# Optimization experiments

Measured on AMD Instinct MI355X. Metric: run time of the kernel, lower is better.

## Reference

```python
import jax, jax.numpy as jnp
import numpy as np

IN_FEATURES = 512
OUT_FEATURES = 512
GRID_SIZE = 8
SPLINE_ORDER = 3


def make_grid():
    # grid has grid_size + 2*spline_order + 1 knots in [-1, 1]
    return jnp.linspace(-1.0, 1.0, GRID_SIZE + 2 * SPLINE_ORDER + 1, dtype=jnp.float32)


def b_splines(x, grid):
    # x: (N, in)  ->  bases: (N, in, grid_size + spline_order)
    x = jnp.clip(x, -2.0, 2.0)[..., None]  # (N, in, 1)
    bases = ((x >= grid[:-1]) & (x < grid[1:])).astype(x.dtype)
    for k in range(1, SPLINE_ORDER + 1):
        denom1 = grid[k:-1] - grid[:-(k + 1)]
        denom1 = jnp.where(jnp.abs(denom1) < 1e-8, jnp.ones_like(denom1), denom1)
        denom2 = grid[k + 1:] - grid[1:-k]
        denom2 = jnp.where(jnp.abs(denom2) < 1e-8, jnp.ones_like(denom2), denom2)
        bases = ((x - grid[:-(k + 1)]) / denom1 * bases[..., :-1]
                 + (grid[k + 1:] - x) / denom2 * bases[..., 1:])
    return bases


def setup_inputs() -> dict:
    key = jax.random.key(0)
    kx, kb, ks = jax.random.split(key, 3)
    x = jax.random.normal(kx, (8192, IN_FEATURES), dtype=jnp.float32)
    # xavier_uniform with gain=0.5 for base_weight
    limit = 0.5 * np.sqrt(6.0 / (IN_FEATURES + OUT_FEATURES))
    base_weight = jax.random.uniform(kb, (OUT_FEATURES, IN_FEATURES), dtype=jnp.float32,
                                     minval=-limit, maxval=limit)
    spline_weight = 0.01 * jax.random.normal(
        ks, (OUT_FEATURES, IN_FEATURES, GRID_SIZE + SPLINE_ORDER), dtype=jnp.float32)
    return {"x": x, "base_weight": base_weight, "spline_weight": spline_weight}


def reference(x, base_weight, spline_weight):
    grid = make_grid()
    base_out = x @ base_weight.T                      # (N, out)
    basis = b_splines(x, grid)                        # (N, in, G+K)
    spline_out = jnp.einsum('bij,oij->bo', basis, spline_weight)
    return base_out + spline_out
```

## Files before the change

kernel.cpp:

```cpp
#include <hip/hip_runtime.h>
#include <stdint.h>

#define IN_F 512
#define OUT_F 512
#define NROWS 8192
#define NSLOT 12
#define KTOT (IN_F * NSLOT)
#define K16S (KTOT / 16)
#define SW_ROW (IN_F * 11)
#define KC_PAD 776
#define AROW 120
#define NGRP 32

typedef __bf16 bf16x8 __attribute__((ext_vector_type(8)));
typedef __bf16 bf16x2 __attribute__((ext_vector_type(2)));
typedef float f32x16 __attribute__((ext_vector_type(16)));

__device__ ushort g_Wb[(K16S * 16 + 1) * 512];

__device__ __forceinline__ ushort f2bf(float f) {
    uint32_t u = __builtin_bit_cast(uint32_t, f);
    u += 0x7FFFu + ((u >> 16) & 1u);
    return (ushort)(u >> 16);
}

__global__ __launch_bounds__(256) void prep_weights(const float* __restrict__ bw,
                                                    const float* __restrict__ sw) {
    __shared__ __align__(16) ushort kcol[16 * KC_PAD];
    const int t  = threadIdx.x;
    const int nt = blockIdx.x & 15;
    const int kg = (blockIdx.x >> 4) & 7;
    const int hv = blockIdx.x >> 7;
    const int o0 = nt * 32 + hv * 16;
    const int f0 = kg * 64;

    {
        const int o_l = t >> 4;
        const int tr  = t & 15;
        const float* swr = sw + (size_t)(o0 + o_l) * SW_ROW + (size_t)f0 * 11;
        #pragma unroll
        for (int i = 0; i < 11; ++i) {
            int p4 = tr + i * 16;
            float4 v = ((const float4*)swr)[p4];
            uint pos = (uint)p4 * 4;
            #pragma unroll
            for (int c = 0; c < 4; ++c) {
                uint pc = pos + c;
                uint fl = pc / 11u;
                uint j  = pc - fl * 11u;
                float val = (c == 0) ? v.x : (c == 1) ? v.y : (c == 2) ? v.z : v.w;
                kcol[o_l * KC_PAD + fl * NSLOT + j] = f2bf(val);
            }
        }
        #pragma unroll
        for (int i = 0; i < 4; ++i) {
            int fl = tr * 4 + i;
            kcol[o_l * KC_PAD + fl * NSLOT + 11] =
                f2bf(bw[(size_t)(o0 + o_l) * IN_F + f0 + fl]);
        }
    }
    __syncthreads();

    {
        const int ol16 = t & 15;
        const int ch   = t >> 4;
        #pragma unroll
        for (int i = 0; i < 6; ++i) {
            int idx  = ch + i * 16;
            int k16l = idx >> 1;
            int hf   = idx & 1;
            uint4 val = *(const uint4*)&kcol[ol16 * KC_PAD + k16l * 16 + hf * 8];
            ((uint4*)g_Wb)[((size_t)nt * K16S + kg * 48 + k16l) * 64 + hf * 32 + hv * 16 + ol16] = val;
        }
    }
}

__device__ __forceinline__ void eval12(float xx, uint p[6]) {
    float wpos = (xx + 1.0f) * 7.0f;
    float fi = floorf(wpos);
    int   i  = (int)fi;
    float u  = wpos - fi;
    bool inr = (xx >= -1.0f) && (xx < 1.0f);
    int   q  = i - 3;
    float um = 1.0f - u;
    float uu = u * u, u3 = uu * u;
    const float C6 = 1.0f / 6.0f;
    float s0 = (inr && q >= 0) ? C6 : 0.0f;
    float s1 = (inr && q >= -1 && q <= 9) ? C6 : 0.0f;
    float s2 = (inr && q >= -2 && q <= 8) ? C6 : 0.0f;
    float s3 = (inr && q <= 7) ? C6 : 0.0f;
    float b0 = um * um * um * s0;
    float b1 = fmaf(3.0f, u3, fmaf(-6.0f, uu, 4.0f)) * s1;
    float b2 = fmaf(-3.0f, u3, fmaf(3.0f, uu, fmaf(3.0f, u, 1.0f))) * s2;
    float b3 = u3 * s3;
    bf16x2 k01; k01[0] = (__bf16)b0; k01[1] = (__bf16)b1;
    bf16x2 k23; k23[0] = (__bf16)b2; k23[1] = (__bf16)b3;
    uint K01 = __builtin_bit_cast(uint, k01);
    uint K23 = __builtin_bit_cast(uint, k23);
    int r  = q & 1;
    int e0 = q & ~1;
    uint P0 = r ? (K01 << 16) : K01;
    uint P1 = r ? ((K01 >> 16) | (K23 << 16)) : K23;
    uint P2 = r ? (K23 >> 16) : 0u;
    #pragma unroll
    for (int pi = 0; pi < 6; ++pi) {
        int d = 2 * pi - e0;
        p[pi] = (d == 0) ? P0 : (d == 2) ? P1 : (d == 4) ? P2 : 0u;
    }
    p[5] = (p[5] & 0xFFFFu) | ((uint)f2bf(xx) << 16);
}

__device__ __forceinline__ void stage4(float4 xv, ushort* dst) {
    uint p[4][6];
    eval12(xv.x, p[0]);
    eval12(xv.y, p[1]);
    eval12(xv.z, p[2]);
    eval12(xv.w, p[3]);
    uint4* d4 = (uint4*)dst;
    d4[0] = make_uint4(p[0][0], p[0][1], p[0][2], p[0][3]);
    d4[1] = make_uint4(p[0][4], p[0][5], p[1][0], p[1][1]);
    d4[2] = make_uint4(p[1][2], p[1][3], p[1][4], p[1][5]);
    d4[3] = make_uint4(p[2][0], p[2][1], p[2][2], p[2][3]);
    d4[4] = make_uint4(p[2][4], p[2][5], p[3][0], p[3][1]);
    d4[5] = make_uint4(p[3][2], p[3][3], p[3][4], p[3][5]);
}

__global__ __launch_bounds__(256, 2) void kan_gemm(const float* __restrict__ x,
                                                   float* __restrict__ out) {
    __shared__ __align__(16) ushort As[2][128 * AROW];

    const int t    = threadIdx.x;
    const int lane = t & 63;
    const int wv   = t >> 6;
    const int wr   = wv >> 1;
    const int wc   = wv & 1;
    const int ln31 = lane & 31;
    const int half = lane >> 5;

    const int bx = blockIdx.x;
    const int mb = bx >> 3;
    const int cg = (bx >> 1) & 3;
    const int kp = bx & 1;
    const int row_base = mb * 128;

    const int srow = t >> 1;
    const int fq   = t & 1;
    const float* xp = x + (size_t)(row_base + srow) * IN_F + kp * 256 + fq * 4;
    ushort* const sb0 = &As[0][srow * AROW + fq * 48];
    ushort* const sb1 = &As[1][srow * AROW + fq * 48];

    const int ntg0 = cg * 4 + wc * 2;
    const uint4* Bp0 = (const uint4*)g_Wb + ((size_t)ntg0 * K16S + kp * 192) * 64 + lane;
    const uint4* Bp1 = Bp0 + (size_t)K16S * 64;

    f32x16 acc[2][2] = {};

    float4 xv = *(const float4*)xp;
    stage4(xv, sb0);
    float4 xn = *(const float4*)(xp + 8);
    __syncthreads();

    #pragma unroll 1
    for (int g = 0; g < NGRP; ++g) {
        const int cur = g & 1;
        uint4 breg[6][2];
        #pragma unroll
        for (int ks = 0; ks < 6; ++ks) {
            breg[ks][0] = Bp0[(size_t)(g * 6 + ks) * 64];
            breg[ks][1] = Bp1[(size_t)(g * 6 + ks) * 64];
        }
        const int gf = (g + 2 < NGRP) ? g + 2 : (NGRP - 1);
        float4 xf = *(const float4*)(xp + gf * 8);

        if (g + 1 < NGRP) stage4(xn, cur ? sb0 : sb1);

        const ushort* Ac = As[cur];
        #pragma unroll
        for (int ks = 0; ks < 6; ++ks) {
            uint4 a0 = *(const uint4*)&Ac[(wr * 64 + ln31) * AROW + ks * 16 + half * 8];
            uint4 a1 = *(const uint4*)&Ac[(wr * 64 + 32 + ln31) * AROW + ks * 16 + half * 8];
            bf16x8 af0 = __builtin_bit_cast(bf16x8, a0);
            bf16x8 af1 = __builtin_bit_cast(bf16x8, a1);
            bf16x8 bf0 = __builtin_bit_cast(bf16x8, breg[ks][0]);
            bf16x8 bf1 = __builtin_bit_cast(bf16x8, breg[ks][1]);
            acc[0][0] = __builtin_amdgcn_mfma_f32_32x32x16_bf16(af0, bf0, acc[0][0], 0, 0, 0);
            acc[0][1] = __builtin_amdgcn_mfma_f32_32x32x16_bf16(af0, bf1, acc[0][1], 0, 0, 0);
            acc[1][0] = __builtin_amdgcn_mfma_f32_32x32x16_bf16(af1, bf0, acc[1][0], 0, 0, 0);
            acc[1][1] = __builtin_amdgcn_mfma_f32_32x32x16_bf16(af1, bf1, acc[1][1], 0, 0, 0);
        }

        xn = xf;
        __syncthreads();
    }

    #pragma unroll
    for (int mt = 0; mt < 2; ++mt) {
        #pragma unroll
        for (int nt = 0; nt < 2; ++nt) {
            int rb = row_base + wr * 64 + mt * 32 + 4 * half;
            int cc = cg * 128 + wc * 64 + nt * 32 + ln31;
            #pragma unroll
            for (int reg = 0; reg < 16; ++reg) {
                int rr = rb + (reg & 3) + 8 * (reg >> 2);
                unsafeAtomicAdd(&out[(size_t)rr * OUT_F + cc], acc[mt][nt][reg]);
            }
        }
    }
}

extern "C" void kernel_launch(void* const* d_in, const int* in_sizes, int n_in,
                              void* d_out, int out_size, void* d_ws, size_t ws_size,
                              hipStream_t stream) {
    const float* x  = (const float*)d_in[0];
    const float* bw = (const float*)d_in[1];
    const float* sw = (const float*)d_in[2];
    float* out = (float*)d_out;
    hipMemsetAsync(out, 0, (size_t)out_size * sizeof(float), stream);
    hipLaunchKernelGGL(prep_weights, dim3(256), dim3(256), 0, stream, bw, sw);
    hipLaunchKernelGGL(kan_gemm, dim3(512), dim3(256), 0, stream, x, out);
}
```

Baseline: 170.8 us.

## Split K four ways, single-buffer A tile, fold output zeroing into prep

Raises the split-K factor from 2 to 4, so the GEMM grid doubles to 1024 blocks, each covering 16 K-groups. The A tile drops from double to single buffering, which halves LDS use and lets the launch bound ask for 3 blocks per CU. The cost is two barriers per iteration with no overlap between staging and MFMA. The output memset moves into the prep kernel to save a separate launch, but doubling split-K also doubles the atomic adds to the output.

Result: faster. 165.9 us (-2.8%).

```diff
diff --git a/kernel.cpp b/kernel.cpp
--- a/kernel.cpp
+++ b/kernel.cpp
@@ -10,7 +10,6 @@
 #define SW_ROW (IN_F * 11)
 #define KC_PAD 776
 #define AROW 120
-#define NGRP 32
 
 typedef __bf16 bf16x8 __attribute__((ext_vector_type(8)));
 typedef __bf16 bf16x2 __attribute__((ext_vector_type(2)));
@@ -25,14 +24,23 @@
 }
 
 __global__ __launch_bounds__(256) void prep_weights(const float* __restrict__ bw,
-                                                    const float* __restrict__ sw) {
+                                                    const float* __restrict__ sw,
+                                                    float* __restrict__ out) {
     __shared__ __align__(16) ushort kcol[16 * KC_PAD];
     const int t  = threadIdx.x;
-    const int nt = blockIdx.x & 15;
-    const int kg = (blockIdx.x >> 4) & 7;
-    const int hv = blockIdx.x >> 7;
+    const int b  = blockIdx.x;
+    const int nt = b & 15;
+    const int kg = (b >> 4) & 7;
+    const int hv = b >> 7;
     const int o0 = nt * 32 + hv * 16;
     const int f0 = kg * 64;
+
+    {
+        float4* o4 = (float4*)out;
+        const float4 z = make_float4(0.f, 0.f, 0.f, 0.f);
+        #pragma unroll
+        for (int i = 0; i < 16; ++i) o4[(size_t)b * 4096 + i * 256 + t] = z;
+    }
 
     {
         const int o_l = t >> 4;
@@ -116,18 +124,20 @@
     eval12(xv.y, p[1]);
     eval12(xv.z, p[2]);
     eval12(xv.w, p[3]);
-    uint4* d4 = (uint4*)dst;
-    d4[0] = make_uint4(p[0][0], p[0][1], p[0][2], p[0][3]);
-    d4[1] = make_uint4(p[0][4], p[0][5], p[1][0], p[1][1]);
-    d4[2] = make_uint4(p[1][2], p[1][3], p[1][4], p[1][5]);
-    d4[3] = make_uint4(p[2][0], p[2][1], p[2][2], p[2][3]);
-    d4[4] = make_uint4(p[2][4], p[2][5], p[3][0], p[3][1]);
-    d4[5] = make_uint4(p[3][2], p[3][3], p[3][4], p[3][5]);
-}
-
-__global__ __launch_bounds__(256, 2) void kan_gemm(const float* __restrict__ x,
+    #pragma unroll
+    for (int c = 0; c < 4; ++c) {
+        uint2 w0; w0.x = p[c][0]; w0.y = p[c][1];
+        uint2 w1; w1.x = p[c][2]; w1.y = p[c][3];
+        uint2 w2; w2.x = p[c][4]; w2.y = p[c][5];
+        *(uint2*)&dst[c * 12 + 0] = w0;
+        *(uint2*)&dst[c * 12 + 4] = w1;
+        *(uint2*)&dst[c * 12 + 8] = w2;
+    }
+}
+
+__global__ __launch_bounds__(256, 3) void kan_gemm(const float* __restrict__ x,
                                                    float* __restrict__ out) {
-    __shared__ __align__(16) ushort As[2][128 * AROW];
+    __shared__ __align__(16) ushort As[128 * AROW];
 
     const int t    = threadIdx.x;
     const int lane = t & 63;
@@ -138,47 +148,44 @@
     const int half = lane >> 5;
 
     const int bx = blockIdx.x;
-    const int mb = bx >> 3;
-    const int cg = (bx >> 1) & 3;
-    const int kp = bx & 1;
+    const int mb = bx >> 4;
+    const int cg = (bx >> 2) & 3;
+    const int kp = bx & 3;
     const int row_base = mb * 128;
 
     const int srow = t >> 1;
     const int fq   = t & 1;
-    const float* xp = x + (size_t)(row_base + srow) * IN_F + kp * 256 + fq * 4;
-    ushort* const sb0 = &As[0][srow * AROW + fq * 48];
-    ushort* const sb1 = &As[1][srow * AROW + fq * 48];
+    const float* xp = x + (size_t)(row_base + srow) * IN_F + kp * 128 + fq * 4;
+    ushort* const sb = &As[srow * AROW + fq * 48];
 
     const int ntg0 = cg * 4 + wc * 2;
-    const uint4* Bp0 = (const uint4*)g_Wb + ((size_t)ntg0 * K16S + kp * 192) * 64 + lane;
+    const uint4* Bp0 = (const uint4*)g_Wb + (size_t)ntg0 * K16S * 64 + lane;
     const uint4* Bp1 = Bp0 + (size_t)K16S * 64;
 
     f32x16 acc[2][2] = {};
 
     float4 xv = *(const float4*)xp;
-    stage4(xv, sb0);
-    float4 xn = *(const float4*)(xp + 8);
-    __syncthreads();
 
     #pragma unroll 1
-    for (int g = 0; g < NGRP; ++g) {
-        const int cur = g & 1;
+    for (int gi = 0; gi < 16; ++gi) {
+        const int g = kp * 16 + gi;
         uint4 breg[6][2];
         #pragma unroll
         for (int ks = 0; ks < 6; ++ks) {
             breg[ks][0] = Bp0[(size_t)(g * 6 + ks) * 64];
             breg[ks][1] = Bp1[(size_t)(g * 6 + ks) * 64];
         }
-        const int gf = (g + 2 < NGRP) ? g + 2 : (NGRP - 1);
-        float4 xf = *(const float4*)(xp + gf * 8);
-
-        if (g + 1 < NGRP) stage4(xn, cur ? sb0 : sb1);
-
-        const ushort* Ac = As[cur];
+        const int gn = (gi + 1 < 16) ? gi + 1 : gi;
+        float4 xn = *(const float4*)(xp + gn * 8);
+
+        __syncthreads();
+        stage4(xv, sb);
+        __syncthreads();
+
         #pragma unroll
         for (int ks = 0; ks < 6; ++ks) {
-            uint4 a0 = *(const uint4*)&Ac[(wr * 64 + ln31) * AROW + ks * 16 + half * 8];
-            uint4 a1 = *(const uint4*)&Ac[(wr * 64 + 32 + ln31) * AROW + ks * 16 + half * 8];
+            uint4 a0 = *(const uint4*)&As[(wr * 64 + ln31) * AROW + ks * 16 + half * 8];
+            uint4 a1 = *(const uint4*)&As[(wr * 64 + 32 + ln31) * AROW + ks * 16 + half * 8];
             bf16x8 af0 = __builtin_bit_cast(bf16x8, a0);
             bf16x8 af1 = __builtin_bit_cast(bf16x8, a1);
             bf16x8 bf0 = __builtin_bit_cast(bf16x8, breg[ks][0]);
@@ -188,21 +195,19 @@
             acc[1][0] = __builtin_amdgcn_mfma_f32_32x32x16_bf16(af1, bf0, acc[1][0], 0, 0, 0);
             acc[1][1] = __builtin_amdgcn_mfma_f32_32x32x16_bf16(af1, bf1, acc[1][1], 0, 0, 0);
         }
-
-        xn = xf;
-        __syncthreads();
+        xv = xn;
     }
 
     #pragma unroll
     for (int mt = 0; mt < 2; ++mt) {
         #pragma unroll
-        for (int nt = 0; nt < 2; ++nt) {
+        for (int nt2 = 0; nt2 < 2; ++nt2) {
             int rb = row_base + wr * 64 + mt * 32 + 4 * half;
-            int cc = cg * 128 + wc * 64 + nt * 32 + ln31;
+            int cc = cg * 128 + wc * 64 + nt2 * 32 + ln31;
             #pragma unroll
             for (int reg = 0; reg < 16; ++reg) {
                 int rr = rb + (reg & 3) + 8 * (reg >> 2);
-                unsafeAtomicAdd(&out[(size_t)rr * OUT_F + cc], acc[mt][nt][reg]);
+                unsafeAtomicAdd(&out[(size_t)rr * OUT_F + cc], acc[mt][nt2][reg]);
             }
         }
     }
@@ -215,7 +220,6 @@
     const float* bw = (const float*)d_in[1];
     const float* sw = (const float*)d_in[2];
     float* out = (float*)d_out;
-    hipMemsetAsync(out, 0, (size_t)out_size * sizeof(float), stream);
-    hipLaunchKernelGGL(prep_weights, dim3(256), dim3(256), 0, stream, bw, sw);
-    hipLaunchKernelGGL(kan_gemm, dim3(512), dim3(256), 0, stream, x, out);
-}
+    hipLaunchKernelGGL(prep_weights, dim3(256), dim3(256), 0, stream, bw, sw, out);
+    hipLaunchKernelGGL(kan_gemm, dim3(1024), dim3(256), 0, stream, x, out);
+}
```
